# Kernel optimization log

Hardware: AMD Instinct MI355X
Metric: run time of the kernel (lower is better)

Reference implementation:

```python
import jax, jax.numpy as jnp
import numpy as np

N, E, IN, H = 20000, 50000, 32, 64


def _lin_init(k, fan_in, shape):
    b = 1.0 / np.sqrt(fan_in)
    return jax.random.uniform(k, shape, jnp.float32, -b, b)


def setup_inputs() -> dict:
    key = jax.random.key(0)
    ks = jax.random.split(key, 16)
    inp = {
        "x": jax.random.normal(ks[0], (N, IN), jnp.float32),
        "edge_index": jax.random.randint(ks[1], (2, E), 0, N, dtype=jnp.int32),
        "edge_attr": jax.random.normal(ks[2], (E, 1, 2), jnp.float32),
        # layer 0: edge MLP 2->H->IN*H, root [IN,H], bias [H]
        "w1_0": _lin_init(ks[3], 2, (2, H)),
        "b1_0": _lin_init(ks[4], 2, (H,)),
        "w2_0": _lin_init(ks[5], H, (H, IN * H)),
        "b2_0": _lin_init(ks[6], H, (IN * H,)),
        "root_0": _lin_init(ks[7], IN, (IN, H)),
        "bias_0": _lin_init(ks[8], IN, (H,)),
        # layer 1: edge MLP 2->H->H*H, root [H,H], bias [H]
        "w1_1": _lin_init(ks[9], 2, (2, H)),
        "b1_1": _lin_init(ks[10], 2, (H,)),
        "w2_1": _lin_init(ks[11], H, (H, H * H)),
        "b2_1": _lin_init(ks[12], H, (H * H,)),
        "root_1": _lin_init(ks[13], H, (H, H)),
        "bias_1": _lin_init(ks[14], H, (H,)),
    }
    return inp


def _nnconv(x, src, dst, ea, w1, b1, w2, b2, root, bias, in_c, out_c):
    # per-edge weight matrices from edge-attr MLP: [E, in_c*out_c]
    h = jax.nn.relu(ea @ w1 + b1) @ w2 + b2
    W = h.reshape(-1, in_c, out_c)                     # [E, in, out]
    msg = jnp.einsum('ei,eio->eo', x[src], W)          # gather + per-edge matmul
    agg = jax.ops.segment_sum(msg, dst, num_segments=x.shape[0])  # scatter-add
    return agg + x @ root + bias                       # add aggr (PyG NNConv, aggr='add')


def reference(x, edge_index, edge_attr,
              w1_0, b1_0, w2_0, b2_0, root_0, bias_0,
              w1_1, b1_1, w2_1, b2_1, root_1, bias_1):
    src, dst = edge_index[0], edge_index[1]
    ea = edge_attr.reshape(edge_attr.shape[0], 2)      # [E, 2]
    x = jax.nn.relu(_nnconv(x, src, dst, ea, w1_0, b1_0, w2_0, b2_0, root_0, bias_0, IN, H))
    x = jax.nn.relu(_nnconv(x, src, dst, ea, w1_1, b1_1, w2_1, b2_1, root_1, bias_1, H, H))
    return x
```

## Files before the change

kernel.cpp:

```cpp
#include <hip/hip_runtime.h>

typedef _Float16 v8h __attribute__((ext_vector_type(8)));
typedef float v16f __attribute__((ext_vector_type(16)));

__global__ void prep_bf_both(const float* __restrict__ w2_0, const float* __restrict__ b2_0,
                             _Float16* __restrict__ BF0,
                             const float* __restrict__ w2_1, const float* __restrict__ b2_1,
                             _Float16* __restrict__ BF1) {
    int idx = blockIdx.x * 256 + threadIdx.x;
    const int n0 = 264 * 512;
    const int n1 = 528 * 512;
    const float* w2; const float* b2; _Float16* BF; int IN, rel;
    if (idx < n0)           { w2 = w2_0; b2 = b2_0; BF = BF0; IN = 32; rel = idx; }
    else if (idx < n0 + n1) { w2 = w2_1; b2 = b2_1; BF = BF1; IN = 64; rel = idx - n0; }
    else return;
    int j = rel & 7, lane = (rel >> 3) & 63, f = rel >> 9;
    int nf = f & 1, kk16 = f >> 1;
    int ln = lane & 31, g2 = lane >> 5;
    int k = kk16 * 16 + g2 * 8 + j;
    int ko = k / IN, i = k - ko * IN;
    int o = nf * 32 + ln;
    float v = (ko < 64) ? w2[ko * (IN * 64) + i * 64 + o]
            : (ko == 64 ? b2[i * 64 + o] : 0.f);
    BF[rel] = (_Float16)v;
}

__global__ void node_root_cvt(const float* __restrict__ x, const float* __restrict__ root,
                              const float* __restrict__ bias, float* __restrict__ agg,
                              _Float16* __restrict__ xb, int N) {
    int idx = blockIdx.x * 256 + threadIdx.x;
    if (idx >= N * 64) return;
    int n = idx >> 6, o = idx & 63;
    float s = bias[o];
    const float* xr = x + (size_t)n * 32;
    #pragma unroll 8
    for (int i = 0; i < 32; ++i) s += xr[i] * root[i * 64 + o];
    agg[idx] = s;
    if (o < 32) xb[n * 32 + o] = (_Float16)xr[o];
}

__global__ void mid_kernel(const float* __restrict__ agg0, const float* __restrict__ root1,
                           const float* __restrict__ bias1, _Float16* __restrict__ x1b,
                           float* __restrict__ agg1, int N) {
    int idx = blockIdx.x * 256 + threadIdx.x;
    if (idx >= N * 64) return;
    int n = idx >> 6, o = idx & 63;
    const float* ar = agg0 + (size_t)n * 64;
    float s = bias1[o];
    #pragma unroll 8
    for (int i = 0; i < 64; ++i) s += fmaxf(ar[i], 0.f) * root1[i * 64 + o];
    agg1[idx] = s;
    x1b[idx] = (_Float16)fmaxf(agg0[idx], 0.f);
}

__global__ void final_relu(const float* __restrict__ agg1, float* __restrict__ out, int n) {
    int idx = blockIdx.x * 256 + threadIdx.x;
    if (idx < n) out[idx] = fmaxf(agg1[idx], 0.f);
}

template<int IN_C>
__global__ __launch_bounds__(256, 3)
void edge_gemm(const float* __restrict__ ea,
               const float* __restrict__ w1, const float* __restrict__ b1,
               const _Float16* __restrict__ xb, const _Float16* __restrict__ BF,
               const int* __restrict__ srcI, const int* __restrict__ dstI,
               float* __restrict__ agg, int E) {
    constexpr int PH  = IN_C / 16;
    constexpr int FR  = 4 * PH;
    constexpr int CH  = FR * 512;
    constexpr int LD4 = FR / 4;
    constexpr int NC  = 33;
    constexpr int CPR = IN_C / 8;

    __shared__ __align__(16) _Float16 sh_b[2][CH];
    __shared__ __align__(16) _Float16 sh_x[64][IN_C];
    __shared__ _Float16 sh_r1[64][66];
    __shared__ int sh_dst[64];

    int tid = threadIdx.x;
    int ebase = blockIdx.x * 64;
    int valid = E - ebase; if (valid > 64) valid = 64;

    if (tid < 64) {
        sh_dst[tid] = (tid < valid) ? dstI[ebase + tid] : 0;
        sh_r1[tid][64] = (_Float16)1.f;
        sh_r1[tid][65] = (_Float16)0.f;
    }
    for (int i = tid; i < 64 * 64; i += 256) {
        int e = i >> 6, j = i & 63;
        int ge = (e < valid) ? (ebase + e) : ebase;
        float a0 = ea[ge * 2], a1 = ea[ge * 2 + 1];
        sh_r1[e][j] = (_Float16)fmaxf(a0 * w1[j] + a1 * w1[64 + j] + b1[j], 0.f);
    }
    for (int i = tid; i < 64 * CPR; i += 256) {
        int r = i / CPR, c = i - r * CPR;
        int sidx = (r < valid) ? srcI[ebase + r] : 0;
        *(uint4*)&sh_x[r][c * 8] = *(const uint4*)(xb + (size_t)sidx * IN_C + (size_t)c * 8);
    }
    const uint4* BF4 = (const uint4*)BF;
    uint4 st[LD4];
    #pragma unroll
    for (int q = 0; q < LD4; ++q) st[q] = BF4[(size_t)q * 256 + tid];
    #pragma unroll
    for (int q = 0; q < LD4; ++q) ((uint4*)sh_b[0])[q * 256 + tid] = st[q];
    __syncthreads();

    int wv = tid >> 6, lane = tid & 63, ln = lane & 31, g2 = lane >> 5;
    int mf = wv & 1, nf = wv >> 1;
    int mrow = mf * 32 + ln;

    v8h xs[PH];
    #pragma unroll
    for (int p = 0; p < PH; ++p) xs[p] = *(const v8h*)&sh_x[mrow][p * 16 + g2 * 8];

    v16f acc = {0,0,0,0,0,0,0,0,0,0,0,0,0,0,0,0};

    for (int c = 0; c < NC; ++c) {
        if (c + 1 < NC) {
            size_t base = (size_t)(c + 1) * (CH / 8);
            #pragma unroll
            for (int q = 0; q < LD4; ++q) st[q] = BF4[base + q * 256 + tid];
        }
        const _Float16* bb = sh_b[c & 1];
        #pragma unroll
        for (int dk = 0; dk < 2; ++dk) {
            _Float16 sv = sh_r1[mrow][c * 2 + dk];
            #pragma unroll
            for (int p = 0; p < PH; ++p) {
                int fi = (dk * PH + p) * 2 + nf;
                v8h b = *(const v8h*)(bb + fi * 512 + lane * 8);
                v8h a = xs[p] * sv;
                acc = __builtin_amdgcn_mfma_f32_32x32x16_f16(a, b, acc, 0, 0, 0);
            }
        }
        if (c + 1 < NC) {
            #pragma unroll
            for (int q = 0; q < LD4; ++q) ((uint4*)sh_b[(c + 1) & 1])[q * 256 + tid] = st[q];
        }
        __syncthreads();
    }

    int colbase = nf * 32 + ln;
    #pragma unroll
    for (int r = 0; r < 16; ++r) {
        int row = mf * 32 + 4 * g2 + (r & 3) + 8 * (r >> 2);
        if (row < valid)
            atomicAdd(&agg[(size_t)sh_dst[row] * 64 + colbase], acc[r]);
    }
}

extern "C" void kernel_launch(void* const* d_in, const int* in_sizes, int n_in,
                              void* d_out, int out_size, void* d_ws, size_t ws_size,
                              hipStream_t stream) {
    const float* x      = (const float*)d_in[0];
    const int*   ei     = (const int*)d_in[1];
    const float* ea     = (const float*)d_in[2];
    const float* w1_0   = (const float*)d_in[3];
    const float* b1_0   = (const float*)d_in[4];
    const float* w2_0   = (const float*)d_in[5];
    const float* b2_0   = (const float*)d_in[6];
    const float* root_0 = (const float*)d_in[7];
    const float* bias_0 = (const float*)d_in[8];
    const float* w1_1   = (const float*)d_in[9];
    const float* b1_1   = (const float*)d_in[10];
    const float* w2_1   = (const float*)d_in[11];
    const float* b2_1   = (const float*)d_in[12];
    const float* root_1 = (const float*)d_in[13];
    const float* bias_1 = (const float*)d_in[14];
    float* out = (float*)d_out;

    int N = in_sizes[0] / 32;
    int E = in_sizes[1] / 2;
    const int* srcI = ei;
    const int* dstI = ei + E;

    char* ws = (char*)d_ws;
    size_t off = 0;
    auto carve = [&](size_t bytes) {
        void* p = ws + off;
        off += (bytes + 255) & ~(size_t)255;
        return p;
    };
    _Float16* BF0  = (_Float16*)carve((size_t)264 * 512 * 2);
    _Float16* BF1  = (_Float16*)carve((size_t)528 * 512 * 2);
    _Float16* XB0  = (_Float16*)carve((size_t)N * 32 * 2);
    _Float16* X1B  = (_Float16*)carve((size_t)N * 64 * 2);
    float*    AGG0 = (float*)carve((size_t)N * 64 * 4);
    float*    AGG1 = (float*)carve((size_t)N * 64 * 4);

    int tbf = (264 + 528) * 512;
    prep_bf_both<<<(tbf + 255) / 256, 256, 0, stream>>>(w2_0, b2_0, BF0, w2_1, b2_1, BF1);
    node_root_cvt<<<(N * 64 + 255) / 256, 256, 0, stream>>>(x, root_0, bias_0, AGG0, XB0, N);

    int gblocks = (E + 63) / 64;
    edge_gemm<32><<<gblocks, 256, 0, stream>>>(ea, w1_0, b1_0, XB0, BF0, srcI, dstI, AGG0, E);

    mid_kernel<<<(N * 64 + 255) / 256, 256, 0, stream>>>(AGG0, root_1, bias_1, X1B, AGG1, N);

    edge_gemm<64><<<gblocks, 256, 0, stream>>>(ea, w1_1, b1_1, X1B, BF1, srcI, dstI, AGG1, E);

    final_relu<<<(N * 64 + 255) / 256, 256, 0, stream>>>(AGG1, out, N * 64);
}
```

Measured before the change: 198.8 us.

## Split K across waves, stream B fragments from global into registers, reduce via LDS

After: 187.9 us. -5.5%, faster.

```diff
diff --git a/kernel.cpp b/kernel.cpp
--- a/kernel.cpp
+++ b/kernel.cpp
@@ -66,15 +66,11 @@
                const int* __restrict__ srcI, const int* __restrict__ dstI,
                float* __restrict__ agg, int E) {
     constexpr int PH  = IN_C / 16;
-    constexpr int FR  = 4 * PH;
-    constexpr int CH  = FR * 512;
-    constexpr int LD4 = FR / 4;
-    constexpr int NC  = 33;
     constexpr int CPR = IN_C / 8;
 
-    __shared__ __align__(16) _Float16 sh_b[2][CH];
     __shared__ __align__(16) _Float16 sh_x[64][IN_C];
     __shared__ _Float16 sh_r1[64][66];
+    __shared__ float buf[64][65];
     __shared__ int sh_dst[64];
 
     int tid = threadIdx.x;
@@ -97,55 +93,72 @@
         int sidx = (r < valid) ? srcI[ebase + r] : 0;
         *(uint4*)&sh_x[r][c * 8] = *(const uint4*)(xb + (size_t)sidx * IN_C + (size_t)c * 8);
     }
-    const uint4* BF4 = (const uint4*)BF;
-    uint4 st[LD4];
+    __syncthreads();
+
+    int wv = tid >> 6, lane = tid & 63, ln = lane & 31, g2 = lane >> 5;
+    int nf = wv & 1, kh = wv >> 1;
+
+    v8h xs0[PH], xs1[PH];
     #pragma unroll
-    for (int q = 0; q < LD4; ++q) st[q] = BF4[(size_t)q * 256 + tid];
-    #pragma unroll
-    for (int q = 0; q < LD4; ++q) ((uint4*)sh_b[0])[q * 256 + tid] = st[q];
+    for (int p = 0; p < PH; ++p) {
+        xs0[p] = *(const v8h*)&sh_x[ln][p * 16 + g2 * 8];
+        xs1[p] = *(const v8h*)&sh_x[ln + 32][p * 16 + g2 * 8];
+    }
+
+    v16f acc0 = {0,0,0,0,0,0,0,0,0,0,0,0,0,0,0,0};
+    v16f acc1 = acc0;
+
+    const uint4* bp = (const uint4*)BF + (size_t)nf * 64 + lane;
+    int kb = kh * 33;
+
+    uint4 b[PH], bn[PH];
+    auto LD = [&](uint4 (&d)[PH], int ko) {
+        #pragma unroll
+        for (int p = 0; p < PH; ++p) d[p] = bp[(size_t)(ko * PH + p) * 128];
+    };
+    auto FM = [&](uint4 (&d)[PH], int ko) {
+        _Float16 sv0 = sh_r1[ln][ko];
+        _Float16 sv1 = sh_r1[ln + 32][ko];
+        #pragma unroll
+        for (int p = 0; p < PH; ++p) {
+            v8h bb; __builtin_memcpy(&bb, &d[p], 16);
+            v8h a0 = xs0[p] * sv0;
+            v8h a1 = xs1[p] * sv1;
+            acc0 = __builtin_amdgcn_mfma_f32_32x32x16_f16(a0, bb, acc0, 0, 0, 0);
+            acc1 = __builtin_amdgcn_mfma_f32_32x32x16_f16(a1, bb, acc1, 0, 0, 0);
+        }
+    };
+
+    LD(b, kb);
+    #pragma unroll 1
+    for (int t = 0; t < 16; ++t) {
+        LD(bn, kb + 2 * t + 1);
+        FM(b,  kb + 2 * t);
+        LD(b,  kb + 2 * t + 2);
+        FM(bn, kb + 2 * t + 1);
+    }
+    FM(b, kb + 32);
+
+    int colb = nf * 32 + ln;
+    if (kh == 1) {
+        #pragma unroll
+        for (int r = 0; r < 16; ++r) {
+            int row = 4 * g2 + (r & 3) + 8 * (r >> 2);
+            buf[row][colb]      = acc0[r];
+            buf[row + 32][colb] = acc1[r];
+        }
+    }
     __syncthreads();
-
-    int wv = tid >> 6, lane = tid & 63, ln = lane & 31, g2 = lane >> 5;
-    int mf = wv & 1, nf = wv >> 1;
-    int mrow = mf * 32 + ln;
-
-    v8h xs[PH];
-    #pragma unroll
-    for (int p = 0; p < PH; ++p) xs[p] = *(const v8h*)&sh_x[mrow][p * 16 + g2 * 8];
-
-    v16f acc = {0,0,0,0,0,0,0,0,0,0,0,0,0,0,0,0};
-
-    for (int c = 0; c < NC; ++c) {
-        if (c + 1 < NC) {
-            size_t base = (size_t)(c + 1) * (CH / 8);
-            #pragma unroll
-            for (int q = 0; q < LD4; ++q) st[q] = BF4[base + q * 256 + tid];
+    if (kh == 0) {
+        #pragma unroll
+        for (int r = 0; r < 16; ++r) {
+            int row = 4 * g2 + (r & 3) + 8 * (r >> 2);
+            if (row < valid)
+                atomicAdd(&agg[(size_t)sh_dst[row] * 64 + colb], acc0[r] + buf[row][colb]);
+            int row1 = row + 32;
+            if (row1 < valid)
+                atomicAdd(&agg[(size_t)sh_dst[row1] * 64 + colb], acc1[r] + buf[row1][colb]);
         }
-        const _Float16* bb = sh_b[c & 1];
-        #pragma unroll
-        for (int dk = 0; dk < 2; ++dk) {
-            _Float16 sv = sh_r1[mrow][c * 2 + dk];
-            #pragma unroll
-            for (int p = 0; p < PH; ++p) {
-                int fi = (dk * PH + p) * 2 + nf;
-                v8h b = *(const v8h*)(bb + fi * 512 + lane * 8);
-                v8h a = xs[p] * sv;
-                acc = __builtin_amdgcn_mfma_f32_32x32x16_f16(a, b, acc, 0, 0, 0);
-            }
-        }
-        if (c + 1 < NC) {
-            #pragma unroll
-            for (int q = 0; q < LD4; ++q) ((uint4*)sh_b[(c + 1) & 1])[q * 256 + tid] = st[q];
-        }
-        __syncthreads();
-    }
-
-    int colbase = nf * 32 + ln;
-    #pragma unroll
-    for (int r = 0; r < 16; ++r) {
-        int row = mf * 32 + 4 * g2 + (r & 3) + 8 * (r >> 2);
-        if (row < valid)
-            atomicAdd(&agg[(size_t)sh_dst[row] * 64 + colbase], acc[r]);
     }
 }
 
```
